# Kernel tuning notes

Hardware: AMD Instinct MI355X
Metric: run time of the kernel (lower is better)

## Reference

```python
import jax, jax.numpy as jnp
import numpy as np


def setup_inputs() -> dict:
    key = jax.random.key(0)
    k1, k2, k3 = jax.random.split(key, 3)
    B, T, D = 4, 8192, 1024
    x = jax.random.normal(k1, (B, T, D), dtype=jnp.float32)
    decay = jax.random.normal(k2, (D,), dtype=jnp.float32)
    freq = jax.random.normal(k3, (D,), dtype=jnp.float32)
    return {"x": x, "decay": decay, "freq": freq}


def reference(x, decay, freq):
    B, T, D = x.shape
    t = jnp.arange(T, dtype=jnp.float32)  # [T]
    # learned decaying-cosine kernel, shape [T, D]
    k = jnp.exp(-jnp.abs(decay)[None, :] * t[:, None]) * jnp.cos(freq[None, :] * t[:, None])
    n_fft = 2 * T  # zero-pad to 2T for linear (causal) convolution
    x_f = jnp.fft.rfft(x, n=n_fft, axis=1)          # [B, T+1, D] complex
    k_f = jnp.fft.rfft(k, n=n_fft, axis=0)          # [T+1, D] complex
    y = jnp.fft.irfft(x_f * k_f[None, :, :], n=n_fft, axis=1)
    return y[:, :T, :]
```

## Files before the change

kernel.cpp:

```cpp
#include <hip/hip_runtime.h>
#include <math.h>


#define D_DIM 1024

__global__ __launch_bounds__(256) void carry_kernel(
    const float* __restrict__ x, const float* __restrict__ decay,
    const float* __restrict__ freq, float2* __restrict__ zloc,
    int T, int L, int C) {
  const int c = blockIdx.x;
  const int b = blockIdx.z;
  const int d = blockIdx.y * 512 + threadIdx.x * 2;

  float a0 = fabsf(decay[d]),     w0 = freq[d];
  float a1 = fabsf(decay[d + 1]), w1 = freq[d + 1];
  float e0 = expf(-a0), e1 = expf(-a1);
  float rr0 = e0 * cosf(w0), ri0 = e0 * sinf(w0);
  float rr1 = e1 * cosf(w1), ri1 = e1 * sinf(w1);

  const float2* xp =
      (const float2*)(x + ((size_t)b * T + (size_t)c * L) * D_DIM + d);
  const size_t stride = D_DIM / 2;

  float z0r = 0.f, z0i = 0.f, z1r = 0.f, z1i = 0.f;
  for (int t = 0; t < L; ++t) {
    float2 xv = xp[(size_t)t * stride];
    float n0r = fmaf(rr0, z0r, fmaf(-ri0, z0i, xv.x));
    float n0i = fmaf(rr0, z0i, ri0 * z0r);
    float n1r = fmaf(rr1, z1r, fmaf(-ri1, z1i, xv.y));
    float n1i = fmaf(rr1, z1i, ri1 * z1r);
    z0r = n0r; z0i = n0i; z1r = n1r; z1i = n1i;
  }
  size_t idx = ((size_t)b * C + c) * D_DIM + d;
  zloc[idx]     = make_float2(z0r, z0i);
  zloc[idx + 1] = make_float2(z1r, z1i);
}

__global__ __launch_bounds__(256) void scan_kernel(
    const float* __restrict__ decay, const float* __restrict__ freq,
    const float2* __restrict__ zloc, float2* __restrict__ zin,
    int L, int C) {
  int g = blockIdx.x * blockDim.x + threadIdx.x;
  int b = g >> 10;
  int d = g & (D_DIM - 1);
  float a = fabsf(decay[d]);
  float w = freq[d];
  float fL = (float)L;
  float e = expf(-a * fL);
  float rLr = e * cosf(w * fL), rLi = e * sinf(w * fL);

  float zr = 0.f, zi = 0.f;
  size_t base = (size_t)b * C * D_DIM + d;
  zin[base] = make_float2(0.f, 0.f);
  for (int c = 1; c < C; ++c) {
    float2 zl = zloc[base + (size_t)(c - 1) * D_DIM];
    float nr = fmaf(rLr, zr, fmaf(-rLi, zi, zl.x));
    float ni = fmaf(rLr, zi, fmaf(rLi, zr, zl.y));
    zr = nr; zi = ni;
    zin[base + (size_t)c * D_DIM] = make_float2(zr, zi);
  }
}

__global__ __launch_bounds__(256) void final_kernel(
    const float* __restrict__ x, const float* __restrict__ decay,
    const float* __restrict__ freq, const float2* __restrict__ zin,
    float* __restrict__ y, int T, int L, int C) {
  const int c = blockIdx.x;
  const int b = blockIdx.z;
  const int d = blockIdx.y * 512 + threadIdx.x * 2;

  float a0 = fabsf(decay[d]),     w0 = freq[d];
  float a1 = fabsf(decay[d + 1]), w1 = freq[d + 1];
  float e0 = expf(-a0), e1 = expf(-a1);
  float rr0 = e0 * cosf(w0), ri0 = e0 * sinf(w0);
  float rr1 = e1 * cosf(w1), ri1 = e1 * sinf(w1);

  size_t zbase = ((size_t)b * C + c) * D_DIM + d;
  float2 s0 = zin[zbase], s1 = zin[zbase + 1];
  float z0r = s0.x, z0i = s0.y, z1r = s1.x, z1i = s1.y;

  const size_t off = ((size_t)b * T + (size_t)c * L) * D_DIM + d;
  const float2* xp = (const float2*)(x + off);
  float2* yp = (float2*)(y + off);
  const size_t stride = D_DIM / 2;

  for (int t = 0; t < L; ++t) {
    float2 xv = xp[(size_t)t * stride];
    float n0r = fmaf(rr0, z0r, fmaf(-ri0, z0i, xv.x));
    float n0i = fmaf(rr0, z0i, ri0 * z0r);
    float n1r = fmaf(rr1, z1r, fmaf(-ri1, z1i, xv.y));
    float n1i = fmaf(rr1, z1i, ri1 * z1r);
    z0r = n0r; z0i = n0i; z1r = n1r; z1i = n1i;
    yp[(size_t)t * stride] = make_float2(z0r, z1r);
  }
}

extern "C" void kernel_launch(void* const* d_in, const int* in_sizes, int n_in,
                              void* d_out, int out_size, void* d_ws, size_t ws_size,
                              hipStream_t stream) {
  const float* x     = (const float*)d_in[0];
  const float* decay = (const float*)d_in[1];
  const float* freq  = (const float*)d_in[2];
  float* y = (float*)d_out;

  const int B = 4, T = 8192;

  int C = 128;
  while (C > 1 && (size_t)C * (size_t)(2 * B * D_DIM * sizeof(float2)) > ws_size)
    C >>= 1;
  int L = T / C;

  float2* zloc = (float2*)d_ws;
  float2* zin  = zloc + (size_t)B * C * D_DIM;

  dim3 grid(C, D_DIM / 512, B);
  carry_kernel<<<grid, 256, 0, stream>>>(x, decay, freq, zloc, T, L, C);
  scan_kernel<<<(B * D_DIM) / 256, 256, 0, stream>>>(decay, freq, zloc, zin, L, C);
  final_kernel<<<grid, 256, 0, stream>>>(x, decay, freq, zin, y, T, L, C);
}
```

Measured before the change: 304.0 us.

## Fuse chunk-carry scan into final kernel and widen per-thread channels to four

Removes the separate sequential scan kernel: each final-kernel block now recomputes its incoming state by scanning all preceding chunk carries itself, which drops one launch and the zin buffer. Each thread handles four channels with float4 loads and stores, the grid loses its D-split dimension, and the output uses nontemporal stores. In exchange, later chunks redo up to C-1 carry reads each (quadratic in C, though small), and the grid has half as many blocks with fewer threads per channel group.

```diff
diff --git a/kernel.cpp b/kernel.cpp
--- a/kernel.cpp
+++ b/kernel.cpp
@@ -4,94 +4,116 @@
 
 #define D_DIM 1024
 
+typedef float floatx4 __attribute__((ext_vector_type(4)));
+
+__device__ __forceinline__ void load_r(const float* __restrict__ decay,
+                                       const float* __restrict__ freq, int d,
+                                       float* rr, float* ri, float* aa, float* ww) {
+  float4 dv = *(const float4*)(decay + d);
+  float4 fv = *(const float4*)(freq + d);
+  float a[4] = {dv.x, dv.y, dv.z, dv.w};
+  float w[4] = {fv.x, fv.y, fv.z, fv.w};
+#pragma unroll
+  for (int k = 0; k < 4; ++k) {
+    float ak = fabsf(a[k]);
+    float e = expf(-ak);
+    rr[k] = e * cosf(w[k]);
+    ri[k] = e * sinf(w[k]);
+    aa[k] = ak;
+    ww[k] = w[k];
+  }
+}
+
 __global__ __launch_bounds__(256) void carry_kernel(
     const float* __restrict__ x, const float* __restrict__ decay,
     const float* __restrict__ freq, float2* __restrict__ zloc,
     int T, int L, int C) {
   const int c = blockIdx.x;
-  const int b = blockIdx.z;
-  const int d = blockIdx.y * 512 + threadIdx.x * 2;
+  const int b = blockIdx.y;
+  const int d = threadIdx.x * 4;
 
-  float a0 = fabsf(decay[d]),     w0 = freq[d];
-  float a1 = fabsf(decay[d + 1]), w1 = freq[d + 1];
-  float e0 = expf(-a0), e1 = expf(-a1);
-  float rr0 = e0 * cosf(w0), ri0 = e0 * sinf(w0);
-  float rr1 = e1 * cosf(w1), ri1 = e1 * sinf(w1);
+  float rr[4], ri[4], aa[4], ww[4];
+  load_r(decay, freq, d, rr, ri, aa, ww);
 
-  const float2* xp =
-      (const float2*)(x + ((size_t)b * T + (size_t)c * L) * D_DIM + d);
-  const size_t stride = D_DIM / 2;
+  const float4* xp =
+      (const float4*)(x + ((size_t)b * T + (size_t)c * L) * D_DIM + d);
+  const size_t stride = D_DIM / 4;
 
-  float z0r = 0.f, z0i = 0.f, z1r = 0.f, z1i = 0.f;
+  float zr[4] = {0.f, 0.f, 0.f, 0.f}, zi[4] = {0.f, 0.f, 0.f, 0.f};
+#pragma unroll 4
   for (int t = 0; t < L; ++t) {
-    float2 xv = xp[(size_t)t * stride];
-    float n0r = fmaf(rr0, z0r, fmaf(-ri0, z0i, xv.x));
-    float n0i = fmaf(rr0, z0i, ri0 * z0r);
-    float n1r = fmaf(rr1, z1r, fmaf(-ri1, z1i, xv.y));
-    float n1i = fmaf(rr1, z1i, ri1 * z1r);
-    z0r = n0r; z0i = n0i; z1r = n1r; z1i = n1i;
+    float4 xv = xp[(size_t)t * stride];
+    float xs[4] = {xv.x, xv.y, xv.z, xv.w};
+#pragma unroll
+    for (int k = 0; k < 4; ++k) {
+      float nr = fmaf(rr[k], zr[k], fmaf(-ri[k], zi[k], xs[k]));
+      float ni = fmaf(rr[k], zi[k], ri[k] * zr[k]);
+      zr[k] = nr;
+      zi[k] = ni;
+    }
   }
-  size_t idx = ((size_t)b * C + c) * D_DIM + d;
-  zloc[idx]     = make_float2(z0r, z0i);
-  zloc[idx + 1] = make_float2(z1r, z1i);
-}
 
-__global__ __launch_bounds__(256) void scan_kernel(
-    const float* __restrict__ decay, const float* __restrict__ freq,
-    const float2* __restrict__ zloc, float2* __restrict__ zin,
-    int L, int C) {
-  int g = blockIdx.x * blockDim.x + threadIdx.x;
-  int b = g >> 10;
-  int d = g & (D_DIM - 1);
-  float a = fabsf(decay[d]);
-  float w = freq[d];
-  float fL = (float)L;
-  float e = expf(-a * fL);
-  float rLr = e * cosf(w * fL), rLi = e * sinf(w * fL);
-
-  float zr = 0.f, zi = 0.f;
-  size_t base = (size_t)b * C * D_DIM + d;
-  zin[base] = make_float2(0.f, 0.f);
-  for (int c = 1; c < C; ++c) {
-    float2 zl = zloc[base + (size_t)(c - 1) * D_DIM];
-    float nr = fmaf(rLr, zr, fmaf(-rLi, zi, zl.x));
-    float ni = fmaf(rLr, zi, fmaf(rLi, zr, zl.y));
-    zr = nr; zi = ni;
-    zin[base + (size_t)c * D_DIM] = make_float2(zr, zi);
-  }
+  float4* zp = (float4*)(zloc + ((size_t)b * C + c) * D_DIM + d);
+  zp[0] = make_float4(zr[0], zi[0], zr[1], zi[1]);
+  zp[1] = make_float4(zr[2], zi[2], zr[3], zi[3]);
 }
 
 __global__ __launch_bounds__(256) void final_kernel(
     const float* __restrict__ x, const float* __restrict__ decay,
-    const float* __restrict__ freq, const float2* __restrict__ zin,
+    const float* __restrict__ freq, const float2* __restrict__ zloc,
     float* __restrict__ y, int T, int L, int C) {
   const int c = blockIdx.x;
-  const int b = blockIdx.z;
-  const int d = blockIdx.y * 512 + threadIdx.x * 2;
+  const int b = blockIdx.y;
+  const int d = threadIdx.x * 4;
 
-  float a0 = fabsf(decay[d]),     w0 = freq[d];
-  float a1 = fabsf(decay[d + 1]), w1 = freq[d + 1];
-  float e0 = expf(-a0), e1 = expf(-a1);
-  float rr0 = e0 * cosf(w0), ri0 = e0 * sinf(w0);
-  float rr1 = e1 * cosf(w1), ri1 = e1 * sinf(w1);
+  float rr[4], ri[4], aa[4], ww[4];
+  load_r(decay, freq, d, rr, ri, aa, ww);
 
-  size_t zbase = ((size_t)b * C + c) * D_DIM + d;
-  float2 s0 = zin[zbase], s1 = zin[zbase + 1];
-  float z0r = s0.x, z0i = s0.y, z1r = s1.x, z1i = s1.y;
+  float rLr[4], rLi[4];
+  const float fL = (float)L;
+#pragma unroll
+  for (int k = 0; k < 4; ++k) {
+    float e = expf(-aa[k] * fL);
+    rLr[k] = e * cosf(ww[k] * fL);
+    rLi[k] = e * sinf(ww[k] * fL);
+  }
+
+  float Zr[4] = {0.f, 0.f, 0.f, 0.f}, Zi[4] = {0.f, 0.f, 0.f, 0.f};
+  const float2* zl = zloc + (size_t)b * C * D_DIM + d;
+  for (int j = 0; j < c; ++j) {
+    float4 v0 = *(const float4*)(zl + (size_t)j * D_DIM);
+    float4 v1 = *(const float4*)(zl + (size_t)j * D_DIM + 2);
+    float lr[4] = {v0.x, v0.z, v1.x, v1.z};
+    float li[4] = {v0.y, v0.w, v1.y, v1.w};
+#pragma unroll
+    for (int k = 0; k < 4; ++k) {
+      float nr = fmaf(rLr[k], Zr[k], fmaf(-rLi[k], Zi[k], lr[k]));
+      float ni = fmaf(rLr[k], Zi[k], fmaf(rLi[k], Zr[k], li[k]));
+      Zr[k] = nr;
+      Zi[k] = ni;
+    }
+  }
 
   const size_t off = ((size_t)b * T + (size_t)c * L) * D_DIM + d;
-  const float2* xp = (const float2*)(x + off);
-  float2* yp = (float2*)(y + off);
-  const size_t stride = D_DIM / 2;
+  const float4* xp = (const float4*)(x + off);
+  floatx4* yp = (floatx4*)(y + off);
+  const size_t stride = D_DIM / 4;
 
+  float zr[4] = {Zr[0], Zr[1], Zr[2], Zr[3]};
+  float zi[4] = {Zi[0], Zi[1], Zi[2], Zi[3]};
+#pragma unroll 4
   for (int t = 0; t < L; ++t) {
-    float2 xv = xp[(size_t)t * stride];
-    float n0r = fmaf(rr0, z0r, fmaf(-ri0, z0i, xv.x));
-    float n0i = fmaf(rr0, z0i, ri0 * z0r);
-    float n1r = fmaf(rr1, z1r, fmaf(-ri1, z1i, xv.y));
-    float n1i = fmaf(rr1, z1i, ri1 * z1r);
-    z0r = n0r; z0i = n0i; z1r = n1r; z1i = n1i;
-    yp[(size_t)t * stride] = make_float2(z0r, z1r);
+    float4 xv = xp[(size_t)t * stride];
+    float xs[4] = {xv.x, xv.y, xv.z, xv.w};
+#pragma unroll
+    for (int k = 0; k < 4; ++k) {
+      float nr = fmaf(rr[k], zr[k], fmaf(-ri[k], zi[k], xs[k]));
+      float ni = fmaf(rr[k], zi[k], ri[k] * zr[k]);
+      zr[k] = nr;
+      zi[k] = ni;
+    }
+    floatx4 out = {zr[0], zr[1], zr[2], zr[3]};
+    __builtin_nontemporal_store(out, &yp[(size_t)t * stride]);
   }
 }
 
@@ -106,15 +128,12 @@
   const int B = 4, T = 8192;
 
   int C = 128;
-  while (C > 1 && (size_t)C * (size_t)(2 * B * D_DIM * sizeof(float2)) > ws_size)
-    C >>= 1;
+  while (C > 1 && (size_t)B * C * D_DIM * sizeof(float2) > ws_size) C >>= 1;
   int L = T / C;
 
   float2* zloc = (float2*)d_ws;
-  float2* zin  = zloc + (size_t)B * C * D_DIM;
 
-  dim3 grid(C, D_DIM / 512, B);
+  dim3 grid(C, B);
   carry_kernel<<<grid, 256, 0, stream>>>(x, decay, freq, zloc, T, L, C);
-  scan_kernel<<<(B * D_DIM) / 256, 256, 0, stream>>>(decay, freq, zloc, zin, L, C);
-  final_kernel<<<grid, 256, 0, stream>>>(x, decay, freq, zin, y, T, L, C);
+  final_kernel<<<grid, 256, 0, stream>>>(x, decay, freq, zloc, y, T, L, C);
 }
```

Measured after the change: 267.1 us. 1.14x faster.
